# Kernel tuning notes

Hardware: AMD Instinct MI355X
Metric: run time of the kernel (lower is better)

Reference implementation:

```python
import jax, jax.numpy as jnp
import numpy as np

N_HEAD = 16
N_KV_HEAD = 4
D_HEAD = 128
RMS_EPS = 1.1920929e-07  # torch default eps for fp32 rms_norm


def _rms_norm(x):
    return x * jax.lax.rsqrt(jnp.mean(x * x, axis=-1, keepdims=True) + RMS_EPS)


def _rotary_tables(n_pos, dim):
    # dim = d_head; freq table has dim//2 entries (half of them zero)
    angular_freq = (1.0 / 1024.0) ** jnp.linspace(0.0, 1.0, dim // 4, dtype=jnp.float32)
    angular_freq = jnp.concatenate([angular_freq, jnp.zeros(dim // 4, jnp.float32)])
    theta = jnp.arange(n_pos, dtype=jnp.float32)[:, None] * angular_freq[None, :]
    return jnp.cos(theta), jnp.sin(theta)


def _apply_rotary(x):
    # x: (B, H, T, D). Faithful to source: cos/sin indexed by x.shape[-3] (= H),
    # broadcast over the time axis.
    n = x.shape[-3]
    cos, sin = _rotary_tables(n, x.shape[-1])
    cos = cos[None, :, None, :]
    sin = sin[None, :, None, :]
    xf = x.astype(jnp.float32)
    x1, x2 = jnp.split(xf, 2, axis=-1)
    y1 = x1 * cos + x2 * sin
    y2 = -x1 * sin + x2 * cos
    return jnp.concatenate([y1, y2], axis=-1).astype(x.dtype)


def setup_inputs() -> dict:
    key = jax.random.key(0)
    k1, k2, k3, k4 = jax.random.split(key, 4)
    B, T, C = 2, 2048, 2048
    return {
        "x": jax.random.normal(k1, (B, T, C), jnp.float32),
        "Wq": jax.random.normal(k2, (C, C), jnp.float32) * 0.02,
        "Wkv": jax.random.normal(k3, (2 * N_KV_HEAD * D_HEAD, C), jnp.float32) * 0.02,
        "Wproj": jax.random.normal(k4, (C, C), jnp.float32) * 0.02,
        "tok_masks": jnp.ones((B, T), jnp.int32),
    }


def reference(x, Wq, Wkv, Wproj, tok_masks):
    B, T, C = x.shape
    nh, nkv, dh = N_HEAD, N_KV_HEAD, D_HEAD

    q = (x @ Wq.T).reshape(B, T, nh, dh).transpose(0, 2, 1, 3)          # (B,nh,T,dh)
    kv = x @ Wkv.T                                                       # (B,T,2*nkv*dh)
    k, v = jnp.split(kv, 2, axis=2)
    k = k.reshape(B, T, nkv, dh).transpose(0, 2, 1, 3)                   # (B,nkv,T,dh)
    v = v.reshape(B, T, nkv, dh).transpose(0, 2, 1, 3)

    q, k = _rms_norm(q), _rms_norm(k)
    q, k = _apply_rotary(q), _apply_rotary(k)

    # GQA: repeat kv heads to match query heads
    rep = nh // nkv
    k = jnp.repeat(k, rep, axis=1)
    v = jnp.repeat(v, rep, axis=1)

    scale = 1.0 / jnp.sqrt(jnp.float32(dh))
    scores = jnp.einsum("bhqd,bhkd->bhqk", q, k) * scale                 # (B,nh,T,T)
    causal = jnp.tril(jnp.ones((T, T), bool))
    scores = jnp.where(causal[None, None], scores, -jnp.inf)
    attn = jax.nn.softmax(scores, axis=-1)
    y = jnp.einsum("bhqk,bhkd->bhqd", attn, v)                           # (B,nh,T,dh)
    y = y.transpose(0, 2, 1, 3).reshape(B, T, C)
    y = y @ Wproj.T
    return (y, jnp.float32(0.0))
```

## Files before the change

### kernel.cpp

```cpp
#include <hip/hip_runtime.h>
#include <hip/hip_bf16.h>

#define T_SEQ 2048
#define BATCH 2
#define CDIM  2048
#define NH    16
#define NKV   4
#define DH    128

typedef __attribute__((ext_vector_type(8))) short bfrag;
typedef __attribute__((ext_vector_type(4))) short bhalf;
typedef __attribute__((ext_vector_type(4))) float ffrag;
typedef __hip_bfloat16 bf16;

__device__ __forceinline__ void gll16(const bf16* __restrict__ g, bf16* lds) {
    __builtin_amdgcn_global_load_lds((const __attribute__((address_space(1))) void*)g,
                                     (__attribute__((address_space(3))) void*)lds, 16, 0, 0);
}

__device__ __forceinline__ unsigned cvt_pk_bf16(float lo, float hi) {
    unsigned r;
    asm("v_cvt_pk_bf16_f32 %0, %1, %2" : "=v"(r) : "v"(lo), "v"(hi));
    return r;
}

struct bf16x4 { bf16 a, b, c, d; };
#define N4_X   (BATCH * T_SEQ * CDIM / 4)
#define N4_WQ  (CDIM * CDIM / 4)
#define N4_WKV (2 * NKV * DH * CDIM / 4)
#define N4_WP  (CDIM * CDIM / 4)
__global__ __launch_bounds__(256) void cast_all(
    const float* __restrict__ x, const float* __restrict__ wq,
    const float* __restrict__ wkv, const float* __restrict__ wp,
    bf16* __restrict__ xb, bf16* __restrict__ wqb, bf16* __restrict__ wkvb, bf16* __restrict__ wpb)
{
    int j = blockIdx.x * 256 + threadIdx.x;
    const float* s; bf16* d;
    if (j < N4_X) { s = x; d = xb; }
    else {
        j -= N4_X;
        if (j < N4_WQ) { s = wq; d = wqb; }
        else {
            j -= N4_WQ;
            if (j < N4_WKV) { s = wkv; d = wkvb; }
            else { j -= N4_WKV; if (j >= N4_WP) return; s = wp; d = wpb; }
        }
    }
    float4 f = ((const float4*)s)[j];
    bf16x4 o{__float2bfloat16(f.x), __float2bfloat16(f.y),
             __float2bfloat16(f.z), __float2bfloat16(f.w)};
    ((bf16x4*)d)[j] = o;
}

template<int MODE, int BN>
__device__ __forceinline__ void gemm_body(
    const bf16* __restrict__ A, const bf16* __restrict__ W, int m0, int n0,
    bf16* __restrict__ out0, bf16* __restrict__ out1, float* __restrict__ outf,
    bf16* __restrict__ sA, bf16* __restrict__ sB)
{
    constexpr int NG = BN / 32;

    const int lane = threadIdx.x & 63;
    const int w    = threadIdx.x >> 6;
    const int wm   = w >> 1, wn = w & 1;
    const int lr   = lane & 15, quad = lane >> 4;

    const int pr8  = lane >> 3;
    const int ls   = (lane & 7) ^ pr8;
    const int rloc = 2 * (w * 8 + pr8) + (ls >> 2);
    const int k0s  = (ls & 3) * 8;

    const bf16* Aj0 = A + (size_t)(m0 +      rloc) * CDIM + k0s;
    const bf16* Aj1 = A + (size_t)(m0 + 64 + rloc) * CDIM + k0s;
    const bf16* Bj0 = W + (size_t)(n0 +      rloc) * CDIM + k0s;
    const bf16* Bj1 = W + (size_t)(n0 + 64 + rloc) * CDIM + k0s;
    bf16* dA0 = sA +        w * 512;
    bf16* dA1 = sA + 2048 + w * 512;
    bf16* dB0 = sB +        w * 512;
    bf16* dB1 = sB + 2048 + w * 512;

    const int soff = ((((lr & 1) << 2) | quad) ^ ((lr >> 1) & 7)) << 3;

    ffrag acc[4][NG] = {};
    for (int kk = 0; kk < CDIM; kk += 32) {
        __syncthreads();
        gll16(Aj0 + kk, dA0);
        gll16(Aj1 + kk, dA1);
        gll16(Bj0 + kk, dB0);
        if constexpr (BN == 128) gll16(Bj1 + kk, dB1);
        __syncthreads();

        bfrag af[4], bg[NG];
        #pragma unroll
        for (int f = 0; f < 4; ++f)
            af[f] = *(const bfrag*)&sA[((f * 16 + wm * 8 + (lr >> 1)) << 6) + soff];
        #pragma unroll
        for (int g = 0; g < NG; ++g)
            bg[g] = *(const bfrag*)&sB[((g * 16 + wn * 8 + (lr >> 1)) << 6) + soff];
        #pragma unroll
        for (int f = 0; f < 4; ++f)
            #pragma unroll
            for (int g = 0; g < NG; ++g)
                acc[f][g] = __builtin_amdgcn_mfma_f32_16x16x32_bf16(af[f], bg[g], acc[f][g], 0, 0, 0);
    }

    #pragma unroll
    for (int f = 0; f < 4; ++f) {
        #pragma unroll
        for (int g = 0; g < NG; ++g) {
            #pragma unroll
            for (int i = 0; i < 4; ++i) {
                const int m = m0 + f * 32 + wm * 16 + quad * 4 + i;
                const int n = n0 + g * 32 + wn * 16 + lr;
                const float v = acc[f][g][i];
                if constexpr (MODE == 0) {
                    int b = m >> 11, t = m & (T_SEQ - 1);
                    int h = n >> 7, d = n & (DH - 1);
                    out0[(((size_t)(b * NH + h) * T_SEQ + t) << 7) + d] = __float2bfloat16(v);
                } else if constexpr (MODE == 1) {
                    int b = m >> 11, t = m & (T_SEQ - 1);
                    if (n < NKV * DH) {
                        int h = n >> 7, d = n & (DH - 1);
                        out0[(((size_t)(b * NKV + h) * T_SEQ + t) << 7) + d] = __float2bfloat16(v);
                    } else {
                        int n2 = n - NKV * DH;
                        int h = n2 >> 7, d = n2 & (DH - 1);
                        out1[(((size_t)(b * NKV + h) * DH + d) << 11) + t] = __float2bfloat16(v);
                    }
                } else {
                    outf[(size_t)m * CDIM + n] = v;
                }
            }
        }
    }
}

__global__ __launch_bounds__(256) void gemm_qkv(
    const bf16* __restrict__ A, const bf16* __restrict__ Wq, const bf16* __restrict__ Wkv,
    bf16* __restrict__ q, bf16* __restrict__ k, bf16* __restrict__ vt)
{
    __shared__ __align__(16) bf16 sA[64 * 64];
    __shared__ __align__(16) bf16 sB[64 * 64];
    if (blockIdx.y < 16)
        gemm_body<0, 128>(A, Wq, blockIdx.x * 128, blockIdx.y * 128, q, nullptr, nullptr, sA, sB);
    else
        gemm_body<1, 128>(A, Wkv, blockIdx.x * 128, (blockIdx.y - 16) * 128, k, vt, nullptr, sA, sB);
}

__global__ __launch_bounds__(256) void gemm_proj(
    const bf16* __restrict__ A, const bf16* __restrict__ W, float* __restrict__ outf)
{
    __shared__ __align__(16) bf16 sA[64 * 64];
    __shared__ __align__(16) bf16 sB[32 * 64];
    gemm_body<2, 64>(A, W, blockIdx.x * 128, blockIdx.y * 64, nullptr, nullptr, outf, sA, sB);
    if (blockIdx.x == 0 && blockIdx.y == 0 && threadIdx.x == 0)
        outf[(size_t)BATCH * T_SEQ * CDIM] = 0.0f;
}

#define QROWS (BATCH * NH * T_SEQ)
#define KROWS (BATCH * NKV * T_SEQ)
__global__ __launch_bounds__(256) void normrope_k(bf16* __restrict__ qb, bf16* __restrict__ kb) {
    int row = blockIdx.x * 4 + (threadIdx.x >> 6);
    bf16* bufb; int nheads;
    if (row < QROWS) { bufb = qb; nheads = NH; }
    else { row -= QROWS; bufb = kb; nheads = NKV; }
    const int h = (row >> 11) % nheads;
    bf16* p = bufb + (size_t)row * DH;
    const int d = threadIdx.x & 63;
    float x1 = __bfloat162float(p[d]);
    float x2 = __bfloat162float(p[d + 64]);
    float ss = x1 * x1 + x2 * x2;
    #pragma unroll
    for (int off = 32; off; off >>= 1) ss += __shfl_xor(ss, off);
    float r = rsqrtf(ss * (1.0f / 128.0f) + 1.1920929e-07f);
    x1 *= r; x2 *= r;
    float freq = (d < 32) ? exp2f(-10.0f * (float)d * (1.0f / 31.0f)) : 0.0f;
    float th = (float)h * freq;
    float c, s;
    __sincosf(th, &s, &c);
    p[d]      = __float2bfloat16(x1 * c + x2 * s);
    p[d + 64] = __float2bfloat16(-x1 * s + x2 * c);
}

__global__ __launch_bounds__(512, 2) void attn_k(const bf16* __restrict__ Q, const bf16* __restrict__ K,
                                                 const bf16* __restrict__ VT, bf16* __restrict__ Y)
{
    const int lane = threadIdx.x & 63;
    const int w = threadIdx.x >> 6;
    const int g = w >> 2, wl = w & 3;
    const int p = blockIdx.x, h = blockIdx.y, b = blockIdx.z;
    const int lr = lane & 15, quad = lane >> 4, lk = quad * 8;
    const bf16* Qb = Q  + (size_t)(b * NH  + h)        * T_SEQ * DH;
    const bf16* Kb = K  + (size_t)(b * NKV + (h >> 2)) * T_SEQ * DH;
    const bf16* Vb = VT + (size_t)(b * NKV + (h >> 2)) * DH * T_SEQ;

    __shared__ __align__(16) union ShmU {
        struct { bf16 SK[2][2][32 * 128]; bf16 SV[2][2][128 * 32]; } s;
        ffrag MRG[9 * 4 * 64];
    } shm;

    const int k_r0 = wl * 8 + (lane >> 4);
    const int k_ch = lane & 15;
    const int v_r0 = wl * 32 + (lane >> 2);
    const int v_ch = lane & 3;
    const int vsw = (lr + (lr >> 2)) & 3;
    const float scale = 0.08838834764831845f;

    auto load_v_perm = [&](const bf16* rp) {
        union { bhalf h[2]; bfrag f; } u;
        u.h[0] = *(const bhalf*)(rp + v_ch * 4);
        u.h[1] = *(const bhalf*)(rp + 16 + v_ch * 4);
        return u.f;
    };

    for (int pass = 0; pass < 2; ++pass) {
        const int qb = pass ? (15 - p) : p;
        const int nc = 2 * (qb + 1);
        const int q0 = qb * 128 + wl * 32;

        bfrag qf[2][4];
        #pragma unroll
        for (int t = 0; t < 2; ++t)
            #pragma unroll
            for (int dc = 0; dc < 4; ++dc)
                qf[t][dc] = *(const bfrag*)(Qb + (size_t)(q0 + t * 16 + lr) * DH + dc * 32 + lk);

        float lp[2] = {};
        ffrag o[2][8] = {};

        bfrag kr[2], vr[2];
        {
            const int b0 = g * 32;
            #pragma unroll
            for (int j = 0; j < 2; ++j) {
                kr[j] = *(const bfrag*)(Kb + (size_t)(b0 + k_r0 + j * 4) * DH + k_ch * 8);
                vr[j] = load_v_perm(Vb + (size_t)(v_r0 + j * 16) * T_SEQ + b0);
            }
            #pragma unroll
            for (int j = 0; j < 2; ++j) {
                int krow = k_r0 + j * 4;
                *(bfrag*)&shm.s.SK[g][0][krow * 128 + ((k_ch ^ (krow & 15))) * 8] = kr[j];
                int vrow = v_r0 + j * 16;
                *(bfrag*)&shm.s.SV[g][0][vrow * 32 + ((v_ch ^ ((vrow + (vrow >> 2)) & 3))) * 8] = vr[j];
            }
            if (nc > 1) {
                const int nb = 64 + g * 32;
                #pragma unroll
                for (int j = 0; j < 2; ++j) {
                    kr[j] = *(const bfrag*)(Kb + (size_t)(nb + k_r0 + j * 4) * DH + k_ch * 8);
                    vr[j] = load_v_perm(Vb + (size_t)(v_r0 + j * 16) * T_SEQ + nb);
                }
            }
        }
        __syncthreads();

        for (int c = 0; c < nc; ++c) {
            const int cur = c & 1, nxt = cur ^ 1;
            const int base = c * 64 + g * 32;
            const bf16* SKc = shm.s.SK[g][cur];
            const bf16* SVc = shm.s.SV[g][cur];

            if (c + 1 < nc) {
                #pragma unroll
                for (int j = 0; j < 2; ++j) {
                    int krow = k_r0 + j * 4;
                    *(bfrag*)&shm.s.SK[g][nxt][krow * 128 + ((k_ch ^ (krow & 15))) * 8] = kr[j];
                    int vrow = v_r0 + j * 16;
                    *(bfrag*)&shm.s.SV[g][nxt][vrow * 32 + ((v_ch ^ ((vrow + (vrow >> 2)) & 3))) * 8] = vr[j];
                }
                if (c + 2 < nc) {
                    const int nb = (c + 2) * 64 + g * 32;
                    #pragma unroll
                    for (int j = 0; j < 2; ++j) {
                        kr[j] = *(const bfrag*)(Kb + (size_t)(nb + k_r0 + j * 4) * DH + k_ch * 8);
                        vr[j] = load_v_perm(Vb + (size_t)(v_r0 + j * 16) * T_SEQ + nb);
                    }
                }
            }

            ffrag s2[2][2] = {};
            #pragma unroll
            for (int kt = 0; kt < 2; ++kt)
                #pragma unroll
                for (int dc = 0; dc < 4; ++dc) {
                    bfrag kf = *(const bfrag*)&SKc[(kt * 16 + lr) * 128 + (((dc << 2) | quad) ^ lr) * 8];
                    s2[0][kt] = __builtin_amdgcn_mfma_f32_16x16x32_bf16(kf, qf[0][dc], s2[0][kt], 0, 0, 0);
                    s2[1][kt] = __builtin_amdgcn_mfma_f32_16x16x32_bf16(kf, qf[1][dc], s2[1][kt], 0, 0, 0);
                }

            const bool maskc = (c >= 2 * qb);
            bfrag pf[2];
            #pragma unroll
            for (int t = 0; t < 2; ++t) {
                const int qa = q0 + t * 16 + lr;
                float ev[2][4];
                #pragma unroll
                for (int kt = 0; kt < 2; ++kt)
                    #pragma unroll
                    for (int i = 0; i < 4; ++i) {
                        const int ka = base + kt * 16 + quad * 4 + i;
                        float e = (!maskc || ka <= qa) ? __expf(fmaf(s2[t][kt][i], scale, -16.0f)) : 0.0f;
                        lp[t] += e;
                        ev[kt][i] = e;
                    }
                union { unsigned u[4]; bfrag f; } pu;
                pu.u[0] = cvt_pk_bf16(ev[0][0], ev[0][1]);
                pu.u[1] = cvt_pk_bf16(ev[0][2], ev[0][3]);
                pu.u[2] = cvt_pk_bf16(ev[1][0], ev[1][1]);
                pu.u[3] = cvt_pk_bf16(ev[1][2], ev[1][3]);
                pf[t] = pu.f;
            }

            #pragma unroll
            for (int dt = 0; dt < 8; ++dt) {
                bfrag vf = *(const bfrag*)&SVc[(dt * 16 + lr) * 32 + ((quad ^ vsw)) * 8];
                o[0][dt] = __builtin_amdgcn_mfma_f32_16x16x32_bf16(pf[0], vf, o[0][dt], 0, 0, 0);
                o[1][dt] = __builtin_amdgcn_mfma_f32_16x16x32_bf16(pf[1], vf, o[1][dt], 0, 0, 0);
            }

            __syncthreads();
        }

        __syncthreads();
        #pragma unroll
        for (int t = 0; t < 2; ++t) {
            if (g == 1) {
                #pragma unroll
                for (int d = 0; d < 8; ++d) shm.MRG[(d * 4 + wl) * 64 + lane] = o[t][d];
                ffrag l4 = {lp[t], 0.0f, 0.0f, 0.0f};
                shm.MRG[(8 * 4 + wl) * 64 + lane] = l4;
            }
            __syncthreads();
            if (g == 0) {
                #pragma unroll
                for (int d = 0; d < 8; ++d) o[t][d] += shm.MRG[(d * 4 + wl) * 64 + lane];
                float lsum = lp[t] + shm.MRG[(8 * 4 + wl) * 64 + lane][0];
                lsum += __shfl_xor(lsum, 16);
                lsum += __shfl_xor(lsum, 32);
                float inv[4];
                #pragma unroll
                for (int i = 0; i < 4; ++i)
                    inv[i] = 1.0f / __shfl(lsum, quad * 4 + i);
                #pragma unroll
                for (int dt = 0; dt < 8; ++dt)
                    #pragma unroll
                    for (int i = 0; i < 4; ++i) {
                        int row = q0 + t * 16 + quad * 4 + i;
                        Y[((size_t)(b * T_SEQ) + row) * CDIM + h * DH + dt * 16 + lr] =
                            __float2bfloat16(o[t][dt][i] * inv[i]);
                    }
            }
            __syncthreads();
        }
    }
}

extern "C" void kernel_launch(void* const* d_in, const int* in_sizes, int n_in,
                              void* d_out, int out_size, void* d_ws, size_t ws_size,
                              hipStream_t stream) {
    const float* x     = (const float*)d_in[0];
    const float* Wq    = (const float*)d_in[1];
    const float* Wkv   = (const float*)d_in[2];
    const float* Wproj = (const float*)d_in[3];
    float* out = (float*)d_out;

    char* ws = (char*)d_ws;
    size_t off = 0;
    auto alloc = [&](size_t bytes) { void* p = ws + off; off += (bytes + 255) & ~255ULL; return p; };
    bf16* xb   = (bf16*)alloc((size_t)BATCH * T_SEQ * CDIM * 2);
    bf16* wqb  = (bf16*)alloc((size_t)CDIM * CDIM * 2);
    bf16* wkvb = (bf16*)alloc((size_t)2 * NKV * DH * CDIM * 2);
    bf16* wpb  = (bf16*)alloc((size_t)CDIM * CDIM * 2);
    bf16* qb   = (bf16*)alloc((size_t)BATCH * NH * T_SEQ * DH * 2);
    bf16* kb   = (bf16*)alloc((size_t)BATCH * NKV * T_SEQ * DH * 2);
    bf16* vtb  = (bf16*)alloc((size_t)BATCH * NKV * DH * T_SEQ * 2);
    bf16* y1   = (bf16*)alloc((size_t)BATCH * T_SEQ * CDIM * 2);

    const int total4 = N4_X + N4_WQ + N4_WKV + N4_WP;
    cast_all<<<(total4 + 255) / 256, 256, 0, stream>>>(x, Wq, Wkv, Wproj, xb, wqb, wkvb, wpb);

    gemm_qkv<<<dim3(32, 24), 256, 0, stream>>>(xb, wqb, wkvb, qb, kb, vtb);
    normrope_k<<<(QROWS + KROWS) / 4, 256, 0, stream>>>(qb, kb);
    attn_k<<<dim3(8, NH, BATCH), 512, 0, stream>>>(qb, kb, vtb, y1);
    gemm_proj<<<dim3(32, 32), 256, 0, stream>>>(y1, wpb, out);
}
```

Before: 296.7 us.

## Double attention KV chunk size per group to halve loop iterations and barriers

```diff
diff --git a/kernel.cpp b/kernel.cpp
--- a/kernel.cpp
+++ b/kernel.cpp
@@ -195,27 +195,29 @@
     const bf16* Vb = VT + (size_t)(b * NKV + (h >> 2)) * DH * T_SEQ;
 
     __shared__ __align__(16) union ShmU {
-        struct { bf16 SK[2][2][32 * 128]; bf16 SV[2][2][128 * 32]; } s;
+        struct { bf16 SK[2][2][64 * 128]; bf16 SV[2][2][128 * 64]; } s;
         ffrag MRG[9 * 4 * 64];
     } shm;
 
-    const int k_r0 = wl * 8 + (lane >> 4);
-    const int k_ch = lane & 15;
-    const int v_r0 = wl * 32 + (lane >> 2);
-    const int v_ch = lane & 3;
-    const int vsw = (lr + (lr >> 2)) & 3;
+    const int k_row = wl * 16 + quad;
+    const int k_ch  = lane & 15;
+    const int v_row = wl * 32 + (lane >> 3);
+    const int v_sl  = lane & 7;
+    const int vc    = v_sl ^ (lane >> 3);
+    const int vH    = vc >> 2, vs = vc & 3;
     const float scale = 0.08838834764831845f;
 
-    auto load_v_perm = [&](const bf16* rp) {
-        union { bhalf h[2]; bfrag f; } u;
-        u.h[0] = *(const bhalf*)(rp + v_ch * 4);
-        u.h[1] = *(const bhalf*)(rp + 16 + v_ch * 4);
+    auto load_v = [&](int kbase, int j) {
+        const bf16* rp = Vb + (size_t)(v_row + j * 8) * T_SEQ + kbase;
+        union { bhalf h2[2]; bfrag f; } u;
+        u.h2[0] = *(const bhalf*)(rp + vH * 32 + vs * 4);
+        u.h2[1] = *(const bhalf*)(rp + vH * 32 + 16 + vs * 4);
         return u.f;
     };
 
     for (int pass = 0; pass < 2; ++pass) {
         const int qb = pass ? (15 - p) : p;
-        const int nc = 2 * (qb + 1);
+        const int nc = qb + 1;
         const int q0 = qb * 128 + wl * 32;
 
         bfrag qf[2][4];
@@ -228,27 +230,27 @@
         float lp[2] = {};
         ffrag o[2][8] = {};
 
-        bfrag kr[2], vr[2];
+        bfrag kr[4], vr[4];
         {
-            const int b0 = g * 32;
-            #pragma unroll
-            for (int j = 0; j < 2; ++j) {
-                kr[j] = *(const bfrag*)(Kb + (size_t)(b0 + k_r0 + j * 4) * DH + k_ch * 8);
-                vr[j] = load_v_perm(Vb + (size_t)(v_r0 + j * 16) * T_SEQ + b0);
-            }
-            #pragma unroll
-            for (int j = 0; j < 2; ++j) {
-                int krow = k_r0 + j * 4;
-                *(bfrag*)&shm.s.SK[g][0][krow * 128 + ((k_ch ^ (krow & 15))) * 8] = kr[j];
-                int vrow = v_r0 + j * 16;
-                *(bfrag*)&shm.s.SV[g][0][vrow * 32 + ((v_ch ^ ((vrow + (vrow >> 2)) & 3))) * 8] = vr[j];
+            const int kb0 = g * 64;
+            #pragma unroll
+            for (int j = 0; j < 4; ++j) {
+                kr[j] = *(const bfrag*)(Kb + (size_t)(kb0 + k_row + j * 4) * DH + k_ch * 8);
+                vr[j] = load_v(kb0, j);
+            }
+            #pragma unroll
+            for (int j = 0; j < 4; ++j) {
+                int krow = k_row + j * 4;
+                *(bfrag*)&shm.s.SK[g][0][krow * 128 + ((k_ch ^ (krow & 15)) << 3)] = kr[j];
+                int vrow = v_row + j * 8;
+                *(bfrag*)&shm.s.SV[g][0][vrow * 64 + (v_sl << 3)] = vr[j];
             }
             if (nc > 1) {
-                const int nb = 64 + g * 32;
-                #pragma unroll
-                for (int j = 0; j < 2; ++j) {
-                    kr[j] = *(const bfrag*)(Kb + (size_t)(nb + k_r0 + j * 4) * DH + k_ch * 8);
-                    vr[j] = load_v_perm(Vb + (size_t)(v_r0 + j * 16) * T_SEQ + nb);
+                const int nb = (2 + g) * 64;
+                #pragma unroll
+                for (int j = 0; j < 4; ++j) {
+                    kr[j] = *(const bfrag*)(Kb + (size_t)(nb + k_row + j * 4) * DH + k_ch * 8);
+                    vr[j] = load_v(nb, j);
                 }
             }
         }
@@ -256,46 +258,46 @@
 
         for (int c = 0; c < nc; ++c) {
             const int cur = c & 1, nxt = cur ^ 1;
-            const int base = c * 64 + g * 32;
+            const int base = (2 * c + g) * 64;
             const bf16* SKc = shm.s.SK[g][cur];
             const bf16* SVc = shm.s.SV[g][cur];
 
             if (c + 1 < nc) {
                 #pragma unroll
-                for (int j = 0; j < 2; ++j) {
-                    int krow = k_r0 + j * 4;
-                    *(bfrag*)&shm.s.SK[g][nxt][krow * 128 + ((k_ch ^ (krow & 15))) * 8] = kr[j];
-                    int vrow = v_r0 + j * 16;
-                    *(bfrag*)&shm.s.SV[g][nxt][vrow * 32 + ((v_ch ^ ((vrow + (vrow >> 2)) & 3))) * 8] = vr[j];
+                for (int j = 0; j < 4; ++j) {
+                    int krow = k_row + j * 4;
+                    *(bfrag*)&shm.s.SK[g][nxt][krow * 128 + ((k_ch ^ (krow & 15)) << 3)] = kr[j];
+                    int vrow = v_row + j * 8;
+                    *(bfrag*)&shm.s.SV[g][nxt][vrow * 64 + (v_sl << 3)] = vr[j];
                 }
                 if (c + 2 < nc) {
-                    const int nb = (c + 2) * 64 + g * 32;
+                    const int nb = (2 * (c + 2) + g) * 64;
                     #pragma unroll
-                    for (int j = 0; j < 2; ++j) {
-                        kr[j] = *(const bfrag*)(Kb + (size_t)(nb + k_r0 + j * 4) * DH + k_ch * 8);
-                        vr[j] = load_v_perm(Vb + (size_t)(v_r0 + j * 16) * T_SEQ + nb);
+                    for (int j = 0; j < 4; ++j) {
+                        kr[j] = *(const bfrag*)(Kb + (size_t)(nb + k_row + j * 4) * DH + k_ch * 8);
+                        vr[j] = load_v(nb, j);
                     }
                 }
             }
 
-            ffrag s2[2][2] = {};
-            #pragma unroll
-            for (int kt = 0; kt < 2; ++kt)
+            ffrag s2[2][4] = {};
+            #pragma unroll
+            for (int kt = 0; kt < 4; ++kt)
                 #pragma unroll
                 for (int dc = 0; dc < 4; ++dc) {
-                    bfrag kf = *(const bfrag*)&SKc[(kt * 16 + lr) * 128 + (((dc << 2) | quad) ^ lr) * 8];
+                    bfrag kf = *(const bfrag*)&SKc[(kt * 16 + lr) * 128 + ((((dc << 2) | quad) ^ lr) << 3)];
                     s2[0][kt] = __builtin_amdgcn_mfma_f32_16x16x32_bf16(kf, qf[0][dc], s2[0][kt], 0, 0, 0);
                     s2[1][kt] = __builtin_amdgcn_mfma_f32_16x16x32_bf16(kf, qf[1][dc], s2[1][kt], 0, 0, 0);
                 }
 
-            const bool maskc = (c >= 2 * qb);
-            bfrag pf[2];
+            const bool maskc = (2 * c + g >= 2 * qb);
+            bfrag pf[2][2];
             #pragma unroll
             for (int t = 0; t < 2; ++t) {
                 const int qa = q0 + t * 16 + lr;
-                float ev[2][4];
-                #pragma unroll
-                for (int kt = 0; kt < 2; ++kt)
+                float ev[4][4];
+                #pragma unroll
+                for (int kt = 0; kt < 4; ++kt)
                     #pragma unroll
                     for (int i = 0; i < 4; ++i) {
                         const int ka = base + kt * 16 + quad * 4 + i;
@@ -308,14 +310,23 @@
                 pu.u[1] = cvt_pk_bf16(ev[0][2], ev[0][3]);
                 pu.u[2] = cvt_pk_bf16(ev[1][0], ev[1][1]);
                 pu.u[3] = cvt_pk_bf16(ev[1][2], ev[1][3]);
-                pf[t] = pu.f;
+                pf[t][0] = pu.f;
+                pu.u[0] = cvt_pk_bf16(ev[2][0], ev[2][1]);
+                pu.u[1] = cvt_pk_bf16(ev[2][2], ev[2][3]);
+                pu.u[2] = cvt_pk_bf16(ev[3][0], ev[3][1]);
+                pu.u[3] = cvt_pk_bf16(ev[3][2], ev[3][3]);
+                pf[t][1] = pu.f;
             }
 
             #pragma unroll
             for (int dt = 0; dt < 8; ++dt) {
-                bfrag vf = *(const bfrag*)&SVc[(dt * 16 + lr) * 32 + ((quad ^ vsw)) * 8];
-                o[0][dt] = __builtin_amdgcn_mfma_f32_16x16x32_bf16(pf[0], vf, o[0][dt], 0, 0, 0);
-                o[1][dt] = __builtin_amdgcn_mfma_f32_16x16x32_bf16(pf[1], vf, o[1][dt], 0, 0, 0);
+                const int vrow = dt * 16 + lr;
+                bfrag vf0 = *(const bfrag*)&SVc[vrow * 64 + ((quad ^ (lr & 7)) << 3)];
+                bfrag vf1 = *(const bfrag*)&SVc[vrow * 64 + (((4 | quad) ^ (lr & 7)) << 3)];
+                o[0][dt] = __builtin_amdgcn_mfma_f32_16x16x32_bf16(pf[0][0], vf0, o[0][dt], 0, 0, 0);
+                o[0][dt] = __builtin_amdgcn_mfma_f32_16x16x32_bf16(pf[0][1], vf1, o[0][dt], 0, 0, 0);
+                o[1][dt] = __builtin_amdgcn_mfma_f32_16x16x32_bf16(pf[1][0], vf0, o[1][dt], 0, 0, 0);
+                o[1][dt] = __builtin_amdgcn_mfma_f32_16x16x32_bf16(pf[1][1], vf1, o[1][dt], 0, 0, 0);
             }
 
             __syncthreads();
```

After: 313.3 us. +5.6%, slower.
